# Kernel tuning notes

Measured on AMD Instinct MI355X. Metric: run time of the kernel, lower is better.

## Reference

```python
import jax, jax.numpy as jnp
import numpy as np

LN_EPS = 1e-5
MIN_BW, MAX_BW, BW_FACTOR = 0.1, 10.0, 1.0
BETA = 0.1


def _layernorm(h, g, b):
    mu = jnp.mean(h, axis=-1, keepdims=True)
    var = jnp.mean((h - mu) ** 2, axis=-1, keepdims=True)
    return (h - mu) * jax.lax.rsqrt(var + LN_EPS) * g + b


def _mlp(x, W1, b1, g, beta, W2, b2):
    # Linear -> LayerNorm -> Dropout(eval: identity) -> GELU(exact) -> Linear
    h = x @ W1 + b1
    h = _layernorm(h, g, beta)
    h = jax.nn.gelu(h, approximate=False)
    return h @ W2 + b2


def _normalize(x):
    n = jnp.linalg.norm(x, axis=-1, keepdims=True)
    return x / jnp.maximum(n, 1e-12)


def _bandwidth(x, y):
    # median-heuristic bandwidth on up to 512 samples; no grad through it
    s = min(512, x.shape[0])
    xs, ys = x[:s], y[:s]
    diff = xs[:, None, :] - ys[None, :, :]          # [s, s, K]
    dist_sq = jnp.sum(diff ** 2, axis=-1)
    bw = jnp.sqrt(jnp.median(dist_sq.reshape(-1)) / 2.0) * BW_FACTOR
    return jax.lax.stop_gradient(jnp.clip(bw, MIN_BW, MAX_BW))


def _score_kernel(x, sx, y, sy):
    # 3-term KSD kernel matrix [B, B]
    bw = _bandwidth(x, y)
    bw2 = bw ** 2
    x2 = jnp.sum(x ** 2, axis=-1)
    y2 = jnp.sum(y ** 2, axis=-1)
    dist_sq = jnp.maximum(x2[:, None] + y2[None, :] - 2.0 * (x @ y.T), 0.0)
    k = jnp.exp(-dist_sq / (2.0 * bw2))
    term1 = k * (sx @ sy.T)
    # sum_d (x_i - y_j)_d * sy_jd  = x_i . sy_j - y_j . sy_j
    term2 = (x @ sy.T - jnp.sum(y * sy, axis=-1)[None, :]) * k / bw2
    D = x.shape[-1]
    term3 = dist_sq * k / (bw2 ** 2) - k * D / bw2
    return term1 + term2 + term3


def setup_inputs() -> dict:
    key = jax.random.key(0)
    B, L, D1, H, K = 256, 128, 768, 1024, 256
    ks = jax.random.split(key, 16)

    def w(k, shape):
        return (jax.random.normal(k, shape, dtype=jnp.float32) * 0.02)

    inp = {
        'image_features': jax.random.normal(ks[0], (B, L, D1), dtype=jnp.float32),
        'text_features': jax.random.normal(ks[1], (B, L, D1), dtype=jnp.float32),
        'eps_img': jax.random.normal(ks[2], (B, L, K), dtype=jnp.float32),
        'eps_txt': jax.random.normal(ks[3], (B, L, K), dtype=jnp.float32),
        'attention_mask': jnp.ones((B, L), dtype=jnp.int32),
    }
    # encoders: D1 -> H -> 2K ; score nets: K -> 2K -> K
    for pfx, k1, k2 in (('enc_i', ks[4], ks[5]), ('enc_t', ks[6], ks[7])):
        inp[pfx + '_W1'] = w(k1, (D1, H)); inp[pfx + '_b1'] = jnp.zeros((H,), jnp.float32)
        inp[pfx + '_g'] = jnp.ones((H,), jnp.float32); inp[pfx + '_beta'] = jnp.zeros((H,), jnp.float32)
        inp[pfx + '_W2'] = w(k2, (H, 2 * K)); inp[pfx + '_b2'] = jnp.zeros((2 * K,), jnp.float32)
    for pfx, k1, k2 in (('sc_i', ks[8], ks[9]), ('sc_t', ks[10], ks[11])):
        inp[pfx + '_W1'] = w(k1, (K, 2 * K)); inp[pfx + '_b1'] = jnp.zeros((2 * K,), jnp.float32)
        inp[pfx + '_g'] = jnp.ones((2 * K,), jnp.float32); inp[pfx + '_beta'] = jnp.zeros((2 * K,), jnp.float32)
        inp[pfx + '_W2'] = w(k2, (2 * K, K)); inp[pfx + '_b2'] = jnp.zeros((K,), jnp.float32)
    return inp


def reference(image_features, text_features, attention_mask, eps_img, eps_txt,
              enc_i_W1, enc_i_b1, enc_i_g, enc_i_beta, enc_i_W2, enc_i_b2,
              enc_t_W1, enc_t_b1, enc_t_g, enc_t_beta, enc_t_W2, enc_t_b2,
              sc_i_W1, sc_i_b1, sc_i_g, sc_i_beta, sc_i_W2, sc_i_b2,
              sc_t_W1, sc_t_b1, sc_t_g, sc_t_beta, sc_t_W2, sc_t_b2):
    B = image_features.shape[0]
    img_params = _mlp(image_features, enc_i_W1, enc_i_b1, enc_i_g, enc_i_beta, enc_i_W2, enc_i_b2)
    txt_params = _mlp(text_features, enc_t_W1, enc_t_b1, enc_t_g, enc_t_beta, enc_t_W2, enc_t_b2)
    K = img_params.shape[-1] // 2
    img_mu, img_logvar = img_params[..., :K], img_params[..., K:]
    txt_mu, txt_logvar = txt_params[..., :K], txt_params[..., K:]

    img_z = _normalize(img_mu + eps_img * jnp.exp(0.5 * img_logvar))
    txt_z = _normalize(txt_mu + eps_txt * jnp.exp(0.5 * txt_logvar))

    img_score = _mlp(img_z, sc_i_W1, sc_i_b1, sc_i_g, sc_i_beta, sc_i_W2, sc_i_b2)
    txt_score = _mlp(txt_z, sc_t_W1, sc_t_b1, sc_t_g, sc_t_beta, sc_t_W2, sc_t_b2)

    seq_last = jnp.sum(attention_mask, axis=1).astype(jnp.int32) - 1   # [B]
    bidx = jnp.arange(B)
    xz, yz = img_z[bidx, seq_last], txt_z[bidx, seq_last]
    xs, ys = img_score[bidx, seq_last], txt_score[bidx, seq_last]

    alignment_loss = jnp.mean(_score_kernel(xz, xs, yz, ys))

    kl1 = -0.5 * jnp.sum(1.0 + img_logvar - img_mu ** 2 - jnp.exp(img_logvar), axis=-1)
    kl2 = -0.5 * jnp.sum(1.0 + txt_logvar - txt_mu ** 2 - jnp.exp(txt_logvar), axis=-1)
    kl_loss = (jnp.mean(kl1[bidx, seq_last]) + jnp.mean(kl2[bidx, seq_last])) / 2.0

    total_loss = kl_loss + BETA * alignment_loss
    return total_loss
```

## Files before the change

kernel.cpp:

```cpp
#include <hip/hip_runtime.h>
#include <math.h>

#define Bb   256
#define Lq   128
#define D1   768
#define Hh   1024
#define Kk   256
#define K2v  512

#define OFF_EPSG  0
#define OFF_P     131072
#define OFF_Z     4325376
#define OFF_SCORE 4456448
#define OFF_DIST  4587520
#define OFF_HIST  4653056
#define OFF_SCAL  4661248
#define OFF_YSY   4661256
#define OFF_BF    4661768

#define UB_XG   0
#define UB_HACT 393216
#define UB_ZB   917504
#define UB_WT   1048576
#define WT_EW1I 0
#define WT_EW1T 786432
#define WT_EW2I 1572864
#define WT_EW2T 2097152
#define WT_SW1I 2621440
#define WT_SW1T 2752512
#define WT_SW2I 2883584
#define WT_SW2T 3014656

typedef __attribute__((ext_vector_type(8))) short short8v;
typedef __attribute__((ext_vector_type(4))) float f32x4;

__device__ __forceinline__ float wred(float v){
#pragma unroll
  for (int m = 32; m; m >>= 1) v += __shfl_xor(v, m, 64);
  return v;
}
__device__ __forceinline__ int wredi(int v){
#pragma unroll
  for (int m = 32; m; m >>= 1) v += __shfl_xor(v, m, 64);
  return v;
}
__device__ __forceinline__ float gelu_exact(float x){
  return 0.5f * x * (1.0f + erff(x * 0.70710678118654752f));
}
__device__ __forceinline__ ushort f2b(float f){
  union { float f; unsigned u; } v; v.f = f;
  return (ushort)((v.u + 0x7FFFu + ((v.u >> 16) & 1u)) >> 16);
}

template<int BM,int KCH,int N,int K>
__device__ __forceinline__ void gemm_stage(
    const ushort* __restrict__ A, const ushort* __restrict__ WTi,
    const ushort* __restrict__ WTt, float* __restrict__ P,
    ushort* LS, int tid, int n0, int r0, int kb, int ks)
{
  constexpr int RPW = BM / 64;
  const int lane = tid & 63, wid = tid >> 6;
  const ushort* WT = (r0 >= 256) ? WTt : WTi;

  f32x4 acc[RPW][4];
#pragma unroll
  for (int s = 0; s < RPW; s++)
#pragma unroll
    for (int c = 0; c < 4; c++) acc[s][c] = (f32x4){0.f,0.f,0.f,0.f};

  const int l15 = lane & 15, kg = lane >> 4;
  const int rdswz = (kg * 16) ^ ((l15 & 3) << 4);

  for (int k0 = kb; k0 < kb + KCH; k0 += 32){
    __syncthreads();
    constexpr int NCHK = (BM + 64) * 4;
#pragma unroll
    for (int i = 0; i < NCHK / 256; i++){
      const int q = (i * 256 + tid) * 16;
      const int row = q >> 6, koff = q & 63;
      const ushort* src = (row < BM)
          ? (A  + (size_t)(r0 + row) * K + k0)
          : (WT + (size_t)(n0 + row - BM) * K + k0);
      short8v v = *reinterpret_cast<const short8v*>(
          reinterpret_cast<const char*>(src) + koff);
      const int dq = (q & ~63) | (koff ^ ((row & 3) << 4));
      *reinterpret_cast<short8v*>(reinterpret_cast<char*>(LS) + dq) = v;
    }
    __syncthreads();
    const char* Ab  = reinterpret_cast<const char*>(LS);
    const char* Bbp = reinterpret_cast<const char*>(LS + BM * 32);
    short8v ar[RPW], bc[4];
#pragma unroll
    for (int s = 0; s < RPW; s++){
      const int row = wid * (RPW * 16) + s * 16 + l15;
      ar[s] = *reinterpret_cast<const short8v*>(Ab + row * 64 + rdswz);
    }
#pragma unroll
    for (int c = 0; c < 4; c++){
      const int col = c * 16 + l15;
      bc[c] = *reinterpret_cast<const short8v*>(Bbp + col * 64 + rdswz);
    }
#pragma unroll
    for (int s = 0; s < RPW; s++)
#pragma unroll
      for (int c = 0; c < 4; c++)
        acc[s][c] = __builtin_amdgcn_mfma_f32_16x16x32_bf16(ar[s], bc[c], acc[s][c], 0, 0, 0);
  }
#pragma unroll
  for (int s = 0; s < RPW; s++)
#pragma unroll
    for (int c = 0; c < 4; c++)
#pragma unroll
      for (int r = 0; r < 4; r++){
        const int row = r0 + wid * (RPW * 16) + s * 16 + kg * 4 + r;
        const int col = n0 + c * 16 + l15;
        P[((size_t)ks * 512 + row) * N + col] = acc[s][c][r];
      }
}

template<int BM,int KCH,int N,int K>
__global__ __launch_bounds__(256) void k_mgemm(
    const ushort* __restrict__ A, const ushort* __restrict__ WTi,
    const ushort* __restrict__ WTt, float* __restrict__ P)
{
  __shared__ __align__(16) ushort LS[(BM + 64) * 32];
  gemm_stage<BM,KCH,N,K>(A, WTi, WTt, P, LS, threadIdx.x,
                         blockIdx.x * 64, blockIdx.y * BM,
                         blockIdx.z * KCH, blockIdx.z);
}

__global__ __launch_bounds__(256) void k_prep(
    const float* __restrict__ img, const float* __restrict__ txt,
    const float* __restrict__ epsi, const float* __restrict__ epst,
    const int* __restrict__ mask,
    const float* __restrict__ eW1i, const float* __restrict__ eW1t,
    const float* __restrict__ eW2i, const float* __restrict__ eW2t,
    const float* __restrict__ sW1i, const float* __restrict__ sW1t,
    const float* __restrict__ sW2i, const float* __restrict__ sW2t,
    ushort* __restrict__ xgb, float* __restrict__ epsg, ushort* __restrict__ wt,
    int* __restrict__ ghist, float* __restrict__ scal)
{
  __shared__ float lsf[32][33];
  __shared__ int s_last;
  const int bid = blockIdx.x, t = threadIdx.x;
  if (bid < 256){
    if (t < 8) reinterpret_cast<int4*>(ghist)[bid * 8 + t] = make_int4(0,0,0,0);
    if (bid == 0 && t < 8) scal[t] = 0.0f;
    int s = 0;
    if (t < 32){
      int4 v = reinterpret_cast<const int4*>(mask + bid * Lq)[t];
      s = v.x + v.y + v.z + v.w;
    }
    if (t < 64){
      int tot = wredi(s);
      if (t == 0) s_last = tot - 1;
    }
    __syncthreads();
    const int last = s_last;
    if (t < 192){
      float4 v = reinterpret_cast<const float4*>(img + (size_t)(bid*Lq+last)*D1)[t];
      ushort4 o; o.x=f2b(v.x); o.y=f2b(v.y); o.z=f2b(v.z); o.w=f2b(v.w);
      reinterpret_cast<ushort4*>(xgb + (size_t)bid*D1)[t] = o;
      float4 w = reinterpret_cast<const float4*>(txt + (size_t)(bid*Lq+last)*D1)[t];
      ushort4 q; q.x=f2b(w.x); q.y=f2b(w.y); q.z=f2b(w.z); q.w=f2b(w.w);
      reinterpret_cast<ushort4*>(xgb + (size_t)(Bb+bid)*D1)[t] = q;
    }
    if (t < 64){
      reinterpret_cast<float4*>(epsg + (size_t)bid*Kk)[t] =
        reinterpret_cast<const float4*>(epsi + (size_t)(bid*Lq+last)*Kk)[t];
      reinterpret_cast<float4*>(epsg + (size_t)(Bb+bid)*Kk)[t] =
        reinterpret_cast<const float4*>(epst + (size_t)(bid*Lq+last)*Kk)[t];
    }
    return;
  }
  const int wb = bid - 256;
  const float* src; ushort* dst; int Kd, Nd, ti;
  if      (wb < 768){  src=eW1i; dst=wt+WT_EW1I; Kd=768;  Nd=1024; ti=wb; }
  else if (wb < 1536){ src=eW1t; dst=wt+WT_EW1T; Kd=768;  Nd=1024; ti=wb-768; }
  else if (wb < 2048){ src=eW2i; dst=wt+WT_EW2I; Kd=1024; Nd=512;  ti=wb-1536; }
  else if (wb < 2560){ src=eW2t; dst=wt+WT_EW2T; Kd=1024; Nd=512;  ti=wb-2048; }
  else if (wb < 2688){ src=sW1i; dst=wt+WT_SW1I; Kd=256;  Nd=512;  ti=wb-2560; }
  else if (wb < 2816){ src=sW1t; dst=wt+WT_SW1T; Kd=256;  Nd=512;  ti=wb-2688; }
  else if (wb < 2944){ src=sW2i; dst=wt+WT_SW2I; Kd=512;  Nd=256;  ti=wb-2816; }
  else               { src=sW2t; dst=wt+WT_SW2T; Kd=512;  Nd=256;  ti=wb-2944; }
  const int ntile = Nd / 32;
  const int k0 = (ti / ntile) * 32, n0 = (ti % ntile) * 32;
  const int r = t >> 3, q = t & 7;
  float4 v = reinterpret_cast<const float4*>(src + (size_t)(k0+r)*Nd + n0)[q];
  lsf[r][q*4+0]=v.x; lsf[r][q*4+1]=v.y; lsf[r][q*4+2]=v.z; lsf[r][q*4+3]=v.w;
  __syncthreads();
  ushort4 o;
  o.x = f2b(lsf[q*4+0][r]); o.y = f2b(lsf[q*4+1][r]);
  o.z = f2b(lsf[q*4+2][r]); o.w = f2b(lsf[q*4+3][r]);
  *reinterpret_cast<ushort4*>(dst + (size_t)(n0+r)*Kd + k0 + q*4) = o;
}

template<int NS>
__global__ __launch_bounds__(256) void k_ln1(
    const float* __restrict__ P,
    const float* __restrict__ b1i, const float* __restrict__ b1t,
    const float* __restrict__ gi,  const float* __restrict__ gt,
    const float* __restrict__ bei, const float* __restrict__ bet,
    ushort* __restrict__ hb)
{
  __shared__ float2 wsum[4];
  const int row = blockIdx.x, t = threadIdx.x;
  const float* b1 = row >= 256 ? b1t : b1i;
  const float* g  = row >= 256 ? gt  : gi;
  const float* be = row >= 256 ? bet : bei;
  const float4* P4 = reinterpret_cast<const float4*>(P);
  float4 v = make_float4(0,0,0,0);
#pragma unroll
  for (int s = 0; s < NS; s++){
    float4 p = P4[((size_t)s * 512 + row) * (Hh/4) + t];
    v.x += p.x; v.y += p.y; v.z += p.z; v.w += p.w;
  }
  float4 bb = reinterpret_cast<const float4*>(b1)[t];
  v.x += bb.x; v.y += bb.y; v.z += bb.z; v.w += bb.w;
  float ps = wred(v.x + v.y + v.z + v.w);
  float pq = wred(v.x*v.x + v.y*v.y + v.z*v.z + v.w*v.w);
  if (!(t & 63)) wsum[t >> 6] = make_float2(ps, pq);
  __syncthreads();
  float S = 0, Q = 0;
#pragma unroll
  for (int i = 0; i < 4; i++){ S += wsum[i].x; Q += wsum[i].y; }
  float mean = S * (1.0f/Hh);
  float rstd = rsqrtf(Q * (1.0f/Hh) - mean*mean + 1e-5f);
  float4 gv  = reinterpret_cast<const float4*>(g)[t];
  float4 bev = reinterpret_cast<const float4*>(be)[t];
  ushort4 o;
  o.x = f2b(gelu_exact((v.x - mean)*rstd*gv.x + bev.x));
  o.y = f2b(gelu_exact((v.y - mean)*rstd*gv.y + bev.y));
  o.z = f2b(gelu_exact((v.z - mean)*rstd*gv.z + bev.z));
  o.w = f2b(gelu_exact((v.w - mean)*rstd*gv.w + bev.w));
  reinterpret_cast<ushort4*>(hb)[(size_t)row * 256 + t] = o;
}

template<int NS>
__global__ __launch_bounds__(128) void k_ln2(
    const float* __restrict__ P,
    const float* __restrict__ b1i, const float* __restrict__ b1t,
    const float* __restrict__ gi,  const float* __restrict__ gt,
    const float* __restrict__ bei, const float* __restrict__ bet,
    ushort* __restrict__ hb2)
{
  __shared__ float2 wsum[2];
  const int row = blockIdx.x, t = threadIdx.x;
  const float* b1 = row >= 256 ? b1t : b1i;
  const float* g  = row >= 256 ? gt  : gi;
  const float* be = row >= 256 ? bet : bei;
  const float4* P4 = reinterpret_cast<const float4*>(P);
  float4 v = make_float4(0,0,0,0);
#pragma unroll
  for (int s = 0; s < NS; s++){
    float4 p = P4[((size_t)s * 512 + row) * (K2v/4) + t];
    v.x += p.x; v.y += p.y; v.z += p.z; v.w += p.w;
  }
  float4 bb = reinterpret_cast<const float4*>(b1)[t];
  v.x += bb.x; v.y += bb.y; v.z += bb.z; v.w += bb.w;
  float ps = wred(v.x + v.y + v.z + v.w);
  float pq = wred(v.x*v.x + v.y*v.y + v.z*v.z + v.w*v.w);
  if (!(t & 63)) wsum[t >> 6] = make_float2(ps, pq);
  __syncthreads();
  float S = wsum[0].x + wsum[1].x, Q = wsum[0].y + wsum[1].y;
  float mean = S * (1.0f/K2v);
  float rstd = rsqrtf(Q * (1.0f/K2v) - mean*mean + 1e-5f);
  float4 gv  = reinterpret_cast<const float4*>(g)[t];
  float4 bev = reinterpret_cast<const float4*>(be)[t];
  ushort4 o;
  o.x = f2b(gelu_exact((v.x - mean)*rstd*gv.x + bev.x));
  o.y = f2b(gelu_exact((v.y - mean)*rstd*gv.y + bev.y));
  o.z = f2b(gelu_exact((v.z - mean)*rstd*gv.z + bev.z));
  o.w = f2b(gelu_exact((v.w - mean)*rstd*gv.w + bev.w));
  reinterpret_cast<ushort4*>(hb2)[(size_t)row * 128 + t] = o;
}

template<int NS>
__global__ __launch_bounds__(64) void k_reparam(
    const float* __restrict__ P,
    const float* __restrict__ b2i, const float* __restrict__ b2t,
    const float* __restrict__ epsg, float* __restrict__ z,
    ushort* __restrict__ zb, float* __restrict__ kl)
{
  const int row = blockIdx.x, t = threadIdx.x;
  const float* b2 = row >= 256 ? b2t : b2i;
  const float4* P4 = reinterpret_cast<const float4*>(P);
  float4 mu = make_float4(0,0,0,0), lv = make_float4(0,0,0,0);
#pragma unroll
  for (int s = 0; s < NS; s++){
    float4 a = P4[((size_t)s * 512 + row) * (K2v/4) + t];
    float4 c = P4[((size_t)s * 512 + row) * (K2v/4) + 64 + t];
    mu.x += a.x; mu.y += a.y; mu.z += a.z; mu.w += a.w;
    lv.x += c.x; lv.y += c.y; lv.z += c.z; lv.w += c.w;
  }
  float4 bm = reinterpret_cast<const float4*>(b2)[t];
  float4 bl = reinterpret_cast<const float4*>(b2)[64 + t];
  mu.x += bm.x; mu.y += bm.y; mu.z += bm.z; mu.w += bm.w;
  lv.x += bl.x; lv.y += bl.y; lv.z += bl.z; lv.w += bl.w;
  float4 ev = reinterpret_cast<const float4*>(epsg)[(size_t)row * 64 + t];
  float z0 = mu.x + ev.x * expf(0.5f * lv.x);
  float z1 = mu.y + ev.y * expf(0.5f * lv.y);
  float z2 = mu.z + ev.z * expf(0.5f * lv.z);
  float z3 = mu.w + ev.w * expf(0.5f * lv.w);
  float s2 = wred(z0*z0 + z1*z1 + z2*z2 + z3*z3);
  float klp = (1.0f + lv.x - mu.x*mu.x - expf(lv.x))
            + (1.0f + lv.y - mu.y*mu.y - expf(lv.y))
            + (1.0f + lv.z - mu.z*mu.z - expf(lv.z))
            + (1.0f + lv.w - mu.w*mu.w - expf(lv.w));
  float klt = wred(klp);
  float inv = 1.0f / fmaxf(sqrtf(s2), 1e-12f);
  float4 zv = make_float4(z0*inv, z1*inv, z2*inv, z3*inv);
  reinterpret_cast<float4*>(z)[(size_t)row * 64 + t] = zv;
  ushort4 o; o.x=f2b(zv.x); o.y=f2b(zv.y); o.z=f2b(zv.z); o.w=f2b(zv.w);
  reinterpret_cast<ushort4*>(zb)[(size_t)row * 64 + t] = o;
  if (t == 0) atomicAdd(kl + (row >= 256 ? 1 : 0), -0.5f * klt);
}

__global__ __launch_bounds__(256) void k_sc1dist(
    const ushort* __restrict__ zb, const ushort* __restrict__ WTi,
    const ushort* __restrict__ WTt, float* __restrict__ P,
    const float* __restrict__ z, float* __restrict__ dist, int* __restrict__ ghist)
{
  __shared__ __align__(16) char SM[256*4 + 8192*4];
  const int bid = blockIdx.x, t = threadIdx.x;
  if (bid < 256){
    ushort* LS = reinterpret_cast<ushort*>(SM);
    const int n0 = (bid & 7) * 64;
    const int r0 = ((bid >> 3) & 7) * 64;
    const int ks = bid >> 6;
    gemm_stage<64,64,512,256>(zb, WTi, WTt, P, LS, t, n0, r0, ks * 64, ks);
    return;
  }
  float* xsh = reinterpret_cast<float*>(SM);
  int*   hl  = reinterpret_cast<int*>(SM + 1024);
  const int i = bid - 256, j = t;
  xsh[j] = z[(size_t)i * Kk + j];
#pragma unroll
  for (int k = j; k < 8192; k += 256) hl[k] = 0;
  __syncthreads();
  const float4* y4 = reinterpret_cast<const float4*>(z + (size_t)Bb * Kk);
  const float4* x4 = reinterpret_cast<const float4*>(xsh);
  float acc = 0.0f;
#pragma unroll 4
  for (int d = 0; d < Kk; d += 4){
    float4 xv = x4[d >> 2];
    float4 yv = y4[j * (Kk/4) + (d >> 2)];
    float d0 = xv.x - yv.x, d1 = xv.y - yv.y, d2 = xv.z - yv.z, d3 = xv.w - yv.w;
    acc += d0*d0 + d1*d1 + d2*d2 + d3*d3;
  }
  dist[i * 256 + j] = acc;
  int bin = (int)(acc * 2048.0f);
  bin = bin < 0 ? 0 : (bin > 8191 ? 8191 : bin);
  atomicAdd(&hl[bin], 1);
  __syncthreads();
  for (int k = j; k < 8192; k += 256){
    int c = hl[k];
    if (c) atomicAdd(ghist + k, c);
  }
}

template<int NS>
__global__ __launch_bounds__(256) void k_sum2bw(
    const float* __restrict__ P,
    const float* __restrict__ b2i, const float* __restrict__ b2t,
    const float* __restrict__ z, float* __restrict__ score, float* __restrict__ ysy,
    const int* __restrict__ ghist, float* __restrict__ scal)
{
  const int bid = blockIdx.x, t = threadIdx.x;
  if (bid < 128){
    const int row = bid * 4 + (t >> 6), lane = t & 63;
    const float* b2 = row >= 256 ? b2t : b2i;
    const float4* P4 = reinterpret_cast<const float4*>(P);
    float4 v = make_float4(0,0,0,0);
#pragma unroll
    for (int s = 0; s < NS; s++){
      float4 q = P4[((size_t)s * 512 + row) * (Kk/4) + lane];
      v.x += q.x; v.y += q.y; v.z += q.z; v.w += q.w;
    }
    float4 bb = reinterpret_cast<const float4*>(b2)[lane];
    v.x += bb.x; v.y += bb.y; v.z += bb.z; v.w += bb.w;
    reinterpret_cast<float4*>(score)[(size_t)row * 64 + lane] = v;
    float4 zv = reinterpret_cast<const float4*>(z)[(size_t)row * 64 + lane];
    float yp = wred(zv.x*v.x + zv.y*v.y + zv.z*v.z + zv.w*v.w);
    if (lane == 0) ysy[row] = yp;
    return;
  }
  __shared__ int wt4[4];
  __shared__ int bres[2];
  const int lane = t & 63, w = t >> 6;
  const int base = t * 32;
  int s = 0;
#pragma unroll
  for (int u = 0; u < 32; u++) s += ghist[base + u];
  int sc = s;
#pragma unroll
  for (int m = 1; m < 64; m <<= 1){
    int o = __shfl_up(sc, m, 64);
    if (lane >= m) sc += o;
  }
  if (lane == 63) wt4[w] = sc;
  __syncthreads();
  int off = 0;
  for (int q = 0; q < w; q++) off += wt4[q];
  int cum = sc + off, basex = cum - s;
#pragma unroll
  for (int rr = 0; rr < 2; rr++){
    int rank = 32768 + rr;
    if (basex < rank && cum >= rank){
      int c = basex;
      for (int u = 0; u < 32; u++){
        c += ghist[base + u];
        if (c >= rank){ bres[rr] = base + u; break; }
      }
    }
  }
  __syncthreads();
  if (t == 0){
    float med = 0.5f * ((bres[0] + 0.5f) + (bres[1] + 0.5f)) * (1.0f / 2048.0f);
    float bw = sqrtf(med * 0.5f);
    bw = fminf(fmaxf(bw, 0.1f), 10.0f);
    scal[3] = bw * bw;
  }
}

__global__ __launch_bounds__(256) void k_score(
    const float* __restrict__ z, const float* __restrict__ score,
    const float* __restrict__ dist, const float* __restrict__ ysy,
    float* __restrict__ scal, float* __restrict__ out)
{
  __shared__ __align__(16) float xsh[Kk];
  __shared__ __align__(16) float sxsh[Kk];
  __shared__ float red4[4];
  const int i = blockIdx.x, j = threadIdx.x;
  xsh[j]  = z[(size_t)i * Kk + j];
  sxsh[j] = score[(size_t)i * Kk + j];
  __syncthreads();
  const float bw2 = scal[3];
  const float4* sy4 = reinterpret_cast<const float4*>(score + (size_t)Bb * Kk);
  const float4* x4  = reinterpret_cast<const float4*>(xsh);
  const float4* sx4 = reinterpret_cast<const float4*>(sxsh);
  float ssy = 0, xsy = 0;
#pragma unroll 4
  for (int d = 0; d < Kk; d += 4){
    float4 xv  = x4[d >> 2];
    float4 sxv = sx4[d >> 2];
    float4 syv = sy4[j * (Kk/4) + (d >> 2)];
    ssy += sxv.x*syv.x + sxv.y*syv.y + sxv.z*syv.z + sxv.w*syv.w;
    xsy += xv.x*syv.x + xv.y*syv.y + xv.z*syv.z + xv.w*syv.w;
  }
  float d2 = dist[i * 256 + j];
  float kv = expf(-d2 / (2.0f * bw2));
  float t1 = kv * ssy;
  float t2 = (xsy - ysy[Bb + j]) * kv / bw2;
  float t3 = d2 * kv / (bw2 * bw2) - kv * (float)Kk / bw2;
  float s = wred(t1 + t2 + t3);
  if (!(j & 63)) red4[j >> 6] = s;
  __syncthreads();
  if (j == 0){
    atomicAdd(scal + 2, red4[0] + red4[1] + red4[2] + red4[3]);
    __threadfence();
    int old = atomicAdd(reinterpret_cast<int*>(scal + 4), 1);
    if (old == 255){
      float kli = __int_as_float(atomicAdd(reinterpret_cast<int*>(scal + 0), 0));
      float klt = __int_as_float(atomicAdd(reinterpret_cast<int*>(scal + 1), 0));
      float alg = __int_as_float(atomicAdd(reinterpret_cast<int*>(scal + 2), 0));
      out[0] = 0.5f * (kli + klt) * (1.0f/256.0f) + 0.1f * alg * (1.0f/65536.0f);
    }
  }
}

extern "C" void kernel_launch(void* const* d_in, const int* in_sizes, int n_in,
                              void* d_out, int out_size, void* d_ws, size_t ws_size,
                              hipStream_t stream) {
  (void)in_sizes; (void)n_in; (void)out_size; (void)ws_size;
  const float* img  = (const float*)d_in[0];
  const float* txt  = (const float*)d_in[1];
  const float* epsi = (const float*)d_in[2];
  const float* epst = (const float*)d_in[3];
  const int*   mask = (const int*)d_in[4];
  const float* eW1i = (const float*)d_in[5];
  const float* eb1i = (const float*)d_in[6];
  const float* egi  = (const float*)d_in[7];
  const float* ebei = (const float*)d_in[8];
  const float* eW2i = (const float*)d_in[9];
  const float* eb2i = (const float*)d_in[10];
  const float* eW1t = (const float*)d_in[11];
  const float* eb1t = (const float*)d_in[12];
  const float* egt  = (const float*)d_in[13];
  const float* ebet = (const float*)d_in[14];
  const float* eW2t = (const float*)d_in[15];
  const float* eb2t = (const float*)d_in[16];
  const float* sW1i = (const float*)d_in[17];
  const float* sb1i = (const float*)d_in[18];
  const float* sgi  = (const float*)d_in[19];
  const float* sbei = (const float*)d_in[20];
  const float* sW2i = (const float*)d_in[21];
  const float* sb2i = (const float*)d_in[22];
  const float* sW1t = (const float*)d_in[23];
  const float* sb1t = (const float*)d_in[24];
  const float* sgt  = (const float*)d_in[25];
  const float* sbet = (const float*)d_in[26];
  const float* sW2t = (const float*)d_in[27];
  const float* sb2t = (const float*)d_in[28];

  float*  ws    = (float*)d_ws;
  float*  epsg  = ws + OFF_EPSG;
  float*  P     = ws + OFF_P;
  float*  z     = ws + OFF_Z;
  float*  score = ws + OFF_SCORE;
  float*  dist  = ws + OFF_DIST;
  int*    ghist = (int*)(ws + OFF_HIST);
  float*  scal  = ws + OFF_SCAL;
  float*  ysy   = ws + OFF_YSY;
  ushort* ub    = (ushort*)(ws + OFF_BF);
  ushort* xgb   = ub + UB_XG;
  ushort* hb    = ub + UB_HACT;
  ushort* zb    = ub + UB_ZB;
  ushort* wt    = ub + UB_WT;

  k_prep<<<3328, 256, 0, stream>>>(img, txt, epsi, epst, mask,
                                   eW1i, eW1t, eW2i, eW2t,
                                   sW1i, sW1t, sW2i, sW2t,
                                   xgb, epsg, wt, ghist, scal);
  k_mgemm<128,96,1024,768><<<dim3(16,4,8), 256, 0, stream>>>(xgb, wt+WT_EW1I, wt+WT_EW1T, P);
  k_ln1<8><<<512, 256, 0, stream>>>(P, eb1i, eb1t, egi, egt, ebei, ebet, hb);
  k_mgemm<128,64,512,1024><<<dim3(8,4,16), 256, 0, stream>>>(hb, wt+WT_EW2I, wt+WT_EW2T, P);
  k_reparam<16><<<512, 64, 0, stream>>>(P, eb2i, eb2t, epsg, z, zb, scal);
  k_sc1dist<<<512, 256, 0, stream>>>(zb, wt+WT_SW1I, wt+WT_SW1T, P, z, dist, ghist);
  k_ln2<4><<<512, 128, 0, stream>>>(P, sb1i, sb1t, sgi, sgt, sbei, sbet, hb);
  k_mgemm<64,32,256,512><<<dim3(4,8,16), 256, 0, stream>>>(hb, wt+WT_SW2I, wt+WT_SW2T, P);
  k_sum2bw<16><<<129, 256, 0, stream>>>(P, sb2i, sb2t, z, score, ysy, ghist, scal);
  k_score<<<256, 256, 0, stream>>>(z, score, dist, ysy, scal, (float*)d_out);
}
```

Measured before the change: 94.48 us.

## Fuse split-K GEMMs with LayerNorm, reparam and score-net epilogues into row-block kernels

Replaces the split-K MFMA GEMMs and their separate partial-sum reduction and LayerNorm/GELU kernels with fused kernels. Each block owns 16 full rows, computes the whole output width in registers, and applies bias, LayerNorm, GELU, reparameterisation/KL or the second score-net layer in shared memory. The bandwidth median search is folded into k_score, and the P workspace is removed, so there are fewer launches and no round trips of fp32 partial sums through global memory. In exchange only 32 blocks run the GEMM stages, and B operands are read straight from global memory without LDS staging, which risks low occupancy and latency-bound inner loops.

Result: slower. 158.2 us (+67.5%).

```diff
diff --git a/kernel.cpp b/kernel.cpp
--- a/kernel.cpp
+++ b/kernel.cpp
@@ -9,14 +9,13 @@
 #define K2v  512
 
 #define OFF_EPSG  0
-#define OFF_P     131072
-#define OFF_Z     4325376
-#define OFF_SCORE 4456448
-#define OFF_DIST  4587520
-#define OFF_HIST  4653056
-#define OFF_SCAL  4661248
-#define OFF_YSY   4661256
-#define OFF_BF    4661768
+#define OFF_Z     131072
+#define OFF_SCORE 262144
+#define OFF_DIST  393216
+#define OFF_HIST  458752
+#define OFF_SCAL  466944
+#define OFF_YSY   466952
+#define OFF_BF    467464
 
 #define UB_XG   0
 #define UB_HACT 393216
@@ -50,83 +49,6 @@
 __device__ __forceinline__ ushort f2b(float f){
   union { float f; unsigned u; } v; v.f = f;
   return (ushort)((v.u + 0x7FFFu + ((v.u >> 16) & 1u)) >> 16);
-}
-
-template<int BM,int KCH,int N,int K>
-__device__ __forceinline__ void gemm_stage(
-    const ushort* __restrict__ A, const ushort* __restrict__ WTi,
-    const ushort* __restrict__ WTt, float* __restrict__ P,
-    ushort* LS, int tid, int n0, int r0, int kb, int ks)
-{
-  constexpr int RPW = BM / 64;
-  const int lane = tid & 63, wid = tid >> 6;
-  const ushort* WT = (r0 >= 256) ? WTt : WTi;
-
-  f32x4 acc[RPW][4];
-#pragma unroll
-  for (int s = 0; s < RPW; s++)
-#pragma unroll
-    for (int c = 0; c < 4; c++) acc[s][c] = (f32x4){0.f,0.f,0.f,0.f};
-
-  const int l15 = lane & 15, kg = lane >> 4;
-  const int rdswz = (kg * 16) ^ ((l15 & 3) << 4);
-
-  for (int k0 = kb; k0 < kb + KCH; k0 += 32){
-    __syncthreads();
-    constexpr int NCHK = (BM + 64) * 4;
-#pragma unroll
-    for (int i = 0; i < NCHK / 256; i++){
-      const int q = (i * 256 + tid) * 16;
-      const int row = q >> 6, koff = q & 63;
-      const ushort* src = (row < BM)
-          ? (A  + (size_t)(r0 + row) * K + k0)
-          : (WT + (size_t)(n0 + row - BM) * K + k0);
-      short8v v = *reinterpret_cast<const short8v*>(
-          reinterpret_cast<const char*>(src) + koff);
-      const int dq = (q & ~63) | (koff ^ ((row & 3) << 4));
-      *reinterpret_cast<short8v*>(reinterpret_cast<char*>(LS) + dq) = v;
-    }
-    __syncthreads();
-    const char* Ab  = reinterpret_cast<const char*>(LS);
-    const char* Bbp = reinterpret_cast<const char*>(LS + BM * 32);
-    short8v ar[RPW], bc[4];
-#pragma unroll
-    for (int s = 0; s < RPW; s++){
-      const int row = wid * (RPW * 16) + s * 16 + l15;
-      ar[s] = *reinterpret_cast<const short8v*>(Ab + row * 64 + rdswz);
-    }
-#pragma unroll
-    for (int c = 0; c < 4; c++){
-      const int col = c * 16 + l15;
-      bc[c] = *reinterpret_cast<const short8v*>(Bbp + col * 64 + rdswz);
-    }
-#pragma unroll
-    for (int s = 0; s < RPW; s++)
-#pragma unroll
-      for (int c = 0; c < 4; c++)
-        acc[s][c] = __builtin_amdgcn_mfma_f32_16x16x32_bf16(ar[s], bc[c], acc[s][c], 0, 0, 0);
-  }
-#pragma unroll
-  for (int s = 0; s < RPW; s++)
-#pragma unroll
-    for (int c = 0; c < 4; c++)
-#pragma unroll
-      for (int r = 0; r < 4; r++){
-        const int row = r0 + wid * (RPW * 16) + s * 16 + kg * 4 + r;
-        const int col = n0 + c * 16 + l15;
-        P[((size_t)ks * 512 + row) * N + col] = acc[s][c][r];
-      }
-}
-
-template<int BM,int KCH,int N,int K>
-__global__ __launch_bounds__(256) void k_mgemm(
-    const ushort* __restrict__ A, const ushort* __restrict__ WTi,
-    const ushort* __restrict__ WTt, float* __restrict__ P)
-{
-  __shared__ __align__(16) ushort LS[(BM + 64) * 32];
-  gemm_stage<BM,KCH,N,K>(A, WTi, WTt, P, LS, threadIdx.x,
-                         blockIdx.x * 64, blockIdx.y * BM,
-                         blockIdx.z * KCH, blockIdx.z);
 }
 
 __global__ __launch_bounds__(256) void k_prep(
@@ -195,247 +117,348 @@
   *reinterpret_cast<ushort4*>(dst + (size_t)(n0+r)*Kd + k0 + q*4) = o;
 }
 
-template<int NS>
-__global__ __launch_bounds__(256) void k_ln1(
-    const float* __restrict__ P,
+__global__ __launch_bounds__(1024) void k_enc1(
+    const ushort* __restrict__ xgb,
+    const ushort* __restrict__ WTi, const ushort* __restrict__ WTt,
     const float* __restrict__ b1i, const float* __restrict__ b1t,
     const float* __restrict__ gi,  const float* __restrict__ gt,
     const float* __restrict__ bei, const float* __restrict__ bet,
     ushort* __restrict__ hb)
 {
-  __shared__ float2 wsum[4];
-  const int row = blockIdx.x, t = threadIdx.x;
-  const float* b1 = row >= 256 ? b1t : b1i;
-  const float* g  = row >= 256 ? gt  : gi;
-  const float* be = row >= 256 ? bet : bei;
-  const float4* P4 = reinterpret_cast<const float4*>(P);
-  float4 v = make_float4(0,0,0,0);
-#pragma unroll
-  for (int s = 0; s < NS; s++){
-    float4 p = P4[((size_t)s * 512 + row) * (Hh/4) + t];
-    v.x += p.x; v.y += p.y; v.z += p.z; v.w += p.w;
-  }
-  float4 bb = reinterpret_cast<const float4*>(b1)[t];
-  v.x += bb.x; v.y += bb.y; v.z += bb.z; v.w += bb.w;
-  float ps = wred(v.x + v.y + v.z + v.w);
-  float pq = wred(v.x*v.x + v.y*v.y + v.z*v.z + v.w*v.w);
-  if (!(t & 63)) wsum[t >> 6] = make_float2(ps, pq);
-  __syncthreads();
-  float S = 0, Q = 0;
-#pragma unroll
-  for (int i = 0; i < 4; i++){ S += wsum[i].x; Q += wsum[i].y; }
-  float mean = S * (1.0f/Hh);
-  float rstd = rsqrtf(Q * (1.0f/Hh) - mean*mean + 1e-5f);
-  float4 gv  = reinterpret_cast<const float4*>(g)[t];
-  float4 bev = reinterpret_cast<const float4*>(be)[t];
-  ushort4 o;
-  o.x = f2b(gelu_exact((v.x - mean)*rstd*gv.x + bev.x));
-  o.y = f2b(gelu_exact((v.y - mean)*rstd*gv.y + bev.y));
-  o.z = f2b(gelu_exact((v.z - mean)*rstd*gv.z + bev.z));
-  o.w = f2b(gelu_exact((v.w - mean)*rstd*gv.w + bev.w));
-  reinterpret_cast<ushort4*>(hb)[(size_t)row * 256 + t] = o;
-}
-
-template<int NS>
-__global__ __launch_bounds__(128) void k_ln2(
-    const float* __restrict__ P,
-    const float* __restrict__ b1i, const float* __restrict__ b1t,
-    const float* __restrict__ gi,  const float* __restrict__ gt,
-    const float* __restrict__ bei, const float* __restrict__ bet,
-    ushort* __restrict__ hb2)
+  __shared__ __align__(16) char ALS[16 * 768 * 2];
+  __shared__ float Hf[16][1028];
+  const int tid = threadIdx.x, lane = tid & 63, w = tid >> 6;
+  const int r0 = blockIdx.x * 16;
+  const ushort* WT = (r0 >= 256) ? WTt : WTi;
+  const float* b1 = (r0 >= 256) ? b1t : b1i;
+  const float* g  = (r0 >= 256) ? gt  : gi;
+  const float* be = (r0 >= 256) ? bet : bei;
+
+  for (int q = tid; q < 16 * 96; q += 1024){
+    int m = q / 96, k8 = q % 96;
+    short8v v = *reinterpret_cast<const short8v*>(xgb + (size_t)(r0+m)*D1 + k8*8);
+    int dq = ((k8 >> 2)*16 + m)*64 + (((k8 & 3) << 4) ^ ((m & 3) << 4));
+    *reinterpret_cast<short8v*>(ALS + dq) = v;
+  }
+  __syncthreads();
+  const int l15 = lane & 15, kg = lane >> 4;
+  const int cb = w * 64;
+  f32x4 acc[4];
+#pragma unroll
+  for (int c = 0; c < 4; c++) acc[c] = (f32x4){0.f,0.f,0.f,0.f};
+#pragma unroll 2
+  for (int ks = 0; ks < 24; ks++){
+    short8v av = *reinterpret_cast<const short8v*>(
+        ALS + (ks*16 + l15)*64 + ((kg*16) ^ ((l15 & 3) << 4)));
+#pragma unroll
+    for (int c = 0; c < 4; c++){
+      short8v bv = *reinterpret_cast<const short8v*>(
+          WT + (size_t)(cb + c*16 + l15)*D1 + ks*32 + kg*8);
+      acc[c] = __builtin_amdgcn_mfma_f32_16x16x32_bf16(av, bv, acc[c], 0, 0, 0);
+    }
+  }
+#pragma unroll
+  for (int c = 0; c < 4; c++){
+    const int col = cb + c*16 + l15;
+    const float bv = b1[col];
+#pragma unroll
+    for (int r = 0; r < 4; r++) Hf[kg*4 + r][col] = acc[c][r] + bv;
+  }
+  __syncthreads();
+  float s = 0.f, q2 = 0.f;
+#pragma unroll
+  for (int j = 0; j < 16; j++){
+    float x = Hf[w][lane + 64*j];
+    s += x; q2 += x*x;
+  }
+  s = wred(s); q2 = wred(q2);
+  const float mean = s * (1.0f/1024.0f);
+  const float rstd = rsqrtf(q2 * (1.0f/1024.0f) - mean*mean + 1e-5f);
+  const int c0 = lane * 16;
+  short8v o0, o1;
+#pragma unroll
+  for (int j = 0; j < 8; j++){
+    float x0 = (Hf[w][c0+j]   - mean)*rstd*g[c0+j]   + be[c0+j];
+    float x1 = (Hf[w][c0+8+j] - mean)*rstd*g[c0+8+j] + be[c0+8+j];
+    o0[j] = (short)f2b(gelu_exact(x0));
+    o1[j] = (short)f2b(gelu_exact(x1));
+  }
+  *reinterpret_cast<short8v*>(hb + (size_t)(r0+w)*Hh + c0)     = o0;
+  *reinterpret_cast<short8v*>(hb + (size_t)(r0+w)*Hh + c0 + 8) = o1;
+}
+
+__global__ __launch_bounds__(512) void k_enc2(
+    const ushort* __restrict__ hbA,
+    const ushort* __restrict__ WTi, const ushort* __restrict__ WTt,
+    const float* __restrict__ b2i, const float* __restrict__ b2t,
+    const float* __restrict__ epsg,
+    float* __restrict__ z, ushort* __restrict__ zb, float* __restrict__ kl)
 {
-  __shared__ float2 wsum[2];
-  const int row = blockIdx.x, t = threadIdx.x;
-  const float* b1 = row >= 256 ? b1t : b1i;
-  const float* g  = row >= 256 ? gt  : gi;
-  const float* be = row >= 256 ? bet : bei;
-  const float4* P4 = reinterpret_cast<const float4*>(P);
-  float4 v = make_float4(0,0,0,0);
-#pragma unroll
-  for (int s = 0; s < NS; s++){
-    float4 p = P4[((size_t)s * 512 + row) * (K2v/4) + t];
-    v.x += p.x; v.y += p.y; v.z += p.z; v.w += p.w;
-  }
-  float4 bb = reinterpret_cast<const float4*>(b1)[t];
-  v.x += bb.x; v.y += bb.y; v.z += bb.z; v.w += bb.w;
-  float ps = wred(v.x + v.y + v.z + v.w);
-  float pq = wred(v.x*v.x + v.y*v.y + v.z*v.z + v.w*v.w);
-  if (!(t & 63)) wsum[t >> 6] = make_float2(ps, pq);
-  __syncthreads();
-  float S = wsum[0].x + wsum[1].x, Q = wsum[0].y + wsum[1].y;
-  float mean = S * (1.0f/K2v);
-  float rstd = rsqrtf(Q * (1.0f/K2v) - mean*mean + 1e-5f);
-  float4 gv  = reinterpret_cast<const float4*>(g)[t];
-  float4 bev = reinterpret_cast<const float4*>(be)[t];
-  ushort4 o;
-  o.x = f2b(gelu_exact((v.x - mean)*rstd*gv.x + bev.x));
-  o.y = f2b(gelu_exact((v.y - mean)*rstd*gv.y + bev.y));
-  o.z = f2b(gelu_exact((v.z - mean)*rstd*gv.z + bev.z));
-  o.w = f2b(gelu_exact((v.w - mean)*rstd*gv.w + bev.w));
-  reinterpret_cast<ushort4*>(hb2)[(size_t)row * 128 + t] = o;
-}
-
-template<int NS>
-__global__ __launch_bounds__(64) void k_reparam(
-    const float* __restrict__ P,
-    const float* __restrict__ b2i, const float* __restrict__ b2t,
-    const float* __restrict__ epsg, float* __restrict__ z,
-    ushort* __restrict__ zb, float* __restrict__ kl)
+  __shared__ __align__(16) char ALS[16 * 1024 * 2];
+  __shared__ float Hf[16][516];
+  const int tid = threadIdx.x, lane = tid & 63, w = tid >> 6;
+  const int r0 = blockIdx.x * 16;
+  const ushort* WT = (r0 >= 256) ? WTt : WTi;
+  const float* b2 = (r0 >= 256) ? b2t : b2i;
+
+  for (int q = tid; q < 16 * 128; q += 512){
+    int m = q >> 7, k8 = q & 127;
+    short8v v = *reinterpret_cast<const short8v*>(hbA + (size_t)(r0+m)*Hh + k8*8);
+    int dq = ((k8 >> 2)*16 + m)*64 + (((k8 & 3) << 4) ^ ((m & 3) << 4));
+    *reinterpret_cast<short8v*>(ALS + dq) = v;
+  }
+  __syncthreads();
+  const int l15 = lane & 15, kg = lane >> 4;
+  const int cb = w * 64;
+  f32x4 acc[4];
+#pragma unroll
+  for (int c = 0; c < 4; c++) acc[c] = (f32x4){0.f,0.f,0.f,0.f};
+#pragma unroll 2
+  for (int ks = 0; ks < 32; ks++){
+    short8v av = *reinterpret_cast<const short8v*>(
+        ALS + (ks*16 + l15)*64 + ((kg*16) ^ ((l15 & 3) << 4)));
+#pragma unroll
+    for (int c = 0; c < 4; c++){
+      short8v bv = *reinterpret_cast<const short8v*>(
+          WT + (size_t)(cb + c*16 + l15)*Hh + ks*32 + kg*8);
+      acc[c] = __builtin_amdgcn_mfma_f32_16x16x32_bf16(av, bv, acc[c], 0, 0, 0);
+    }
+  }
+#pragma unroll
+  for (int c = 0; c < 4; c++){
+    const int col = cb + c*16 + l15;
+    const float bv = b2[col];
+#pragma unroll
+    for (int r = 0; r < 4; r++) Hf[kg*4 + r][col] = acc[c][r] + bv;
+  }
+  __syncthreads();
+#pragma unroll
+  for (int rr = 0; rr < 2; rr++){
+    const int row = w + rr*8;
+    const int grow = r0 + row;
+    float4 mu = *reinterpret_cast<const float4*>(&Hf[row][lane*4]);
+    float4 lv = *reinterpret_cast<const float4*>(&Hf[row][256 + lane*4]);
+    float4 ev = reinterpret_cast<const float4*>(epsg + (size_t)grow*Kk)[lane];
+    float z0 = mu.x + ev.x * expf(0.5f * lv.x);
+    float z1 = mu.y + ev.y * expf(0.5f * lv.y);
+    float z2 = mu.z + ev.z * expf(0.5f * lv.z);
+    float z3 = mu.w + ev.w * expf(0.5f * lv.w);
+    float s2 = wred(z0*z0 + z1*z1 + z2*z2 + z3*z3);
+    float klp = (1.0f + lv.x - mu.x*mu.x - expf(lv.x))
+              + (1.0f + lv.y - mu.y*mu.y - expf(lv.y))
+              + (1.0f + lv.z - mu.z*mu.z - expf(lv.z))
+              + (1.0f + lv.w - mu.w*mu.w - expf(lv.w));
+    float klt = wred(klp);
+    float inv = 1.0f / fmaxf(sqrtf(s2), 1e-12f);
+    float4 zv = make_float4(z0*inv, z1*inv, z2*inv, z3*inv);
+    reinterpret_cast<float4*>(z)[(size_t)grow * 64 + lane] = zv;
+    ushort4 o; o.x=f2b(zv.x); o.y=f2b(zv.y); o.z=f2b(zv.z); o.w=f2b(zv.w);
+    reinterpret_cast<ushort4*>(zb)[(size_t)grow * 64 + lane] = o;
+    if (lane == 0) atomicAdd(kl + (grow >= 256 ? 1 : 0), -0.5f * klt);
+  }
+}
+
+__global__ __launch_bounds__(512) void k_sc(
+    const ushort* __restrict__ zb,
+    const ushort* __restrict__ W1i, const ushort* __restrict__ W1t,
+    const float* __restrict__ sb1i, const float* __restrict__ sb1t,
+    const float* __restrict__ sgi,  const float* __restrict__ sgt,
+    const float* __restrict__ sbei, const float* __restrict__ sbet,
+    const ushort* __restrict__ W2i, const ushort* __restrict__ W2t,
+    const float* __restrict__ sb2i, const float* __restrict__ sb2t,
+    const float* __restrict__ z, float* __restrict__ score, float* __restrict__ ysy,
+    float* __restrict__ dist, int* __restrict__ ghist)
 {
-  const int row = blockIdx.x, t = threadIdx.x;
-  const float* b2 = row >= 256 ? b2t : b2i;
-  const float4* P4 = reinterpret_cast<const float4*>(P);
-  float4 mu = make_float4(0,0,0,0), lv = make_float4(0,0,0,0);
-#pragma unroll
-  for (int s = 0; s < NS; s++){
-    float4 a = P4[((size_t)s * 512 + row) * (K2v/4) + t];
-    float4 c = P4[((size_t)s * 512 + row) * (K2v/4) + 64 + t];
-    mu.x += a.x; mu.y += a.y; mu.z += a.z; mu.w += a.w;
-    lv.x += c.x; lv.y += c.y; lv.z += c.z; lv.w += c.w;
-  }
-  float4 bm = reinterpret_cast<const float4*>(b2)[t];
-  float4 bl = reinterpret_cast<const float4*>(b2)[64 + t];
-  mu.x += bm.x; mu.y += bm.y; mu.z += bm.z; mu.w += bm.w;
-  lv.x += bl.x; lv.y += bl.y; lv.z += bl.z; lv.w += bl.w;
-  float4 ev = reinterpret_cast<const float4*>(epsg)[(size_t)row * 64 + t];
-  float z0 = mu.x + ev.x * expf(0.5f * lv.x);
-  float z1 = mu.y + ev.y * expf(0.5f * lv.y);
-  float z2 = mu.z + ev.z * expf(0.5f * lv.z);
-  float z3 = mu.w + ev.w * expf(0.5f * lv.w);
-  float s2 = wred(z0*z0 + z1*z1 + z2*z2 + z3*z3);
-  float klp = (1.0f + lv.x - mu.x*mu.x - expf(lv.x))
-            + (1.0f + lv.y - mu.y*mu.y - expf(lv.y))
-            + (1.0f + lv.z - mu.z*mu.z - expf(lv.z))
-            + (1.0f + lv.w - mu.w*mu.w - expf(lv.w));
-  float klt = wred(klp);
-  float inv = 1.0f / fmaxf(sqrtf(s2), 1e-12f);
-  float4 zv = make_float4(z0*inv, z1*inv, z2*inv, z3*inv);
-  reinterpret_cast<float4*>(z)[(size_t)row * 64 + t] = zv;
-  ushort4 o; o.x=f2b(zv.x); o.y=f2b(zv.y); o.z=f2b(zv.z); o.w=f2b(zv.w);
-  reinterpret_cast<ushort4*>(zb)[(size_t)row * 64 + t] = o;
-  if (t == 0) atomicAdd(kl + (row >= 256 ? 1 : 0), -0.5f * klt);
-}
-
-__global__ __launch_bounds__(256) void k_sc1dist(
-    const ushort* __restrict__ zb, const ushort* __restrict__ WTi,
-    const ushort* __restrict__ WTt, float* __restrict__ P,
-    const float* __restrict__ z, float* __restrict__ dist, int* __restrict__ ghist)
-{
-  __shared__ __align__(16) char SM[256*4 + 8192*4];
-  const int bid = blockIdx.x, t = threadIdx.x;
-  if (bid < 256){
-    ushort* LS = reinterpret_cast<ushort*>(SM);
-    const int n0 = (bid & 7) * 64;
-    const int r0 = ((bid >> 3) & 7) * 64;
-    const int ks = bid >> 6;
-    gemm_stage<64,64,512,256>(zb, WTi, WTt, P, LS, t, n0, r0, ks * 64, ks);
+  __shared__ __align__(16) char SM[74240];
+  const int bid = blockIdx.x, tid = threadIdx.x;
+  const int lane = tid & 63, w = tid >> 6;
+  if (bid < 32){
+    char* ALS = SM;
+    float (*Hf)[516] = reinterpret_cast<float(*)[516]>(SM + 8192);
+    char* HK = SM + 8192 + 33024;
+    float (*SF)[260] = reinterpret_cast<float(*)[260]>(SM + 57600);
+    const int r0 = bid * 16;
+    const ushort* W1 = (r0 >= 256) ? W1t : W1i;
+    const float* b1 = (r0 >= 256) ? sb1t : sb1i;
+    const float* g  = (r0 >= 256) ? sgt  : sgi;
+    const float* be = (r0 >= 256) ? sbet : sbei;
+    const ushort* W2 = (r0 >= 256) ? W2t : W2i;
+    const float* b2 = (r0 >= 256) ? sb2t : sb2i;
+
+    {
+      int q = tid;
+      int m = q >> 5, k8 = q & 31;
+      short8v v = *reinterpret_cast<const short8v*>(zb + (size_t)(r0+m)*Kk + k8*8);
+      int dq = ((k8 >> 2)*16 + m)*64 + (((k8 & 3) << 4) ^ ((m & 3) << 4));
+      *reinterpret_cast<short8v*>(ALS + dq) = v;
+    }
+    __syncthreads();
+    const int l15 = lane & 15, kg = lane >> 4;
+    {
+      const int cb = w * 64;
+      f32x4 acc[4];
+#pragma unroll
+      for (int c = 0; c < 4; c++) acc[c] = (f32x4){0.f,0.f,0.f,0.f};
+#pragma unroll
+      for (int ks = 0; ks < 8; ks++){
+        short8v av = *reinterpret_cast<const short8v*>(
+            ALS + (ks*16 + l15)*64 + ((kg*16) ^ ((l15 & 3) << 4)));
+#pragma unroll
+        for (int c = 0; c < 4; c++){
+          short8v bv = *reinterpret_cast<const short8v*>(
+              W1 + (size_t)(cb + c*16 + l15)*Kk + ks*32 + kg*8);
+          acc[c] = __builtin_amdgcn_mfma_f32_16x16x32_bf16(av, bv, acc[c], 0, 0, 0);
+        }
+      }
+#pragma unroll
+      for (int c = 0; c < 4; c++){
+        const int col = cb + c*16 + l15;
+        const float bv = b1[col];
+#pragma unroll
+        for (int r = 0; r < 4; r++) Hf[kg*4 + r][col] = acc[c][r] + bv;
+      }
+    }
+    __syncthreads();
+#pragma unroll
+    for (int rr = 0; rr < 2; rr++){
+      const int row = w + rr*8;
+      float s = 0.f, q2 = 0.f;
+#pragma unroll
+      for (int j = 0; j < 8; j++){
+        float x = Hf[row][lane + 64*j];
+        s += x; q2 += x*x;
+      }
+      s = wred(s); q2 = wred(q2);
+      const float mean = s * (1.0f/512.0f);
+      const float rstd = rsqrtf(q2 * (1.0f/512.0f) - mean*mean + 1e-5f);
+      const int c0 = lane * 8;
+      short8v o;
+#pragma unroll
+      for (int j = 0; j < 8; j++){
+        float x = (Hf[row][c0+j] - mean)*rstd*g[c0+j] + be[c0+j];
+        o[j] = (short)f2b(gelu_exact(x));
+      }
+      int dq = ((lane >> 2)*16 + row)*64 + (((lane & 3) << 4) ^ ((row & 3) << 4));
+      *reinterpret_cast<short8v*>(HK + dq) = o;
+    }
+    __syncthreads();
+    {
+      const int cw = w * 32;
+      f32x4 acc[2];
+      acc[0] = (f32x4){0.f,0.f,0.f,0.f}; acc[1] = (f32x4){0.f,0.f,0.f,0.f};
+#pragma unroll 2
+      for (int ks = 0; ks < 16; ks++){
+        short8v av = *reinterpret_cast<const short8v*>(
+            HK + (ks*16 + l15)*64 + ((kg*16) ^ ((l15 & 3) << 4)));
+#pragma unroll
+        for (int c = 0; c < 2; c++){
+          short8v bv = *reinterpret_cast<const short8v*>(
+              W2 + (size_t)(cw + c*16 + l15)*K2v + ks*32 + kg*8);
+          acc[c] = __builtin_amdgcn_mfma_f32_16x16x32_bf16(av, bv, acc[c], 0, 0, 0);
+        }
+      }
+#pragma unroll
+      for (int c = 0; c < 2; c++){
+        const int col = cw + c*16 + l15;
+        const float bv = b2[col];
+#pragma unroll
+        for (int r = 0; r < 4; r++) SF[kg*4 + r][col] = acc[c][r] + bv;
+      }
+    }
+    __syncthreads();
+#pragma unroll
+    for (int rr = 0; rr < 2; rr++){
+      const int row = w + rr*8;
+      const int grow = r0 + row;
+      float4 sv = *reinterpret_cast<const float4*>(&SF[row][lane*4]);
+      reinterpret_cast<float4*>(score)[(size_t)grow * 64 + lane] = sv;
+      float4 zv = reinterpret_cast<const float4*>(z)[(size_t)grow * 64 + lane];
+      float yp = wred(zv.x*sv.x + zv.y*sv.y + zv.z*sv.z + zv.w*sv.w);
+      if (lane == 0) ysy[grow] = yp;
+    }
     return;
   }
-  float* xsh = reinterpret_cast<float*>(SM);
-  int*   hl  = reinterpret_cast<int*>(SM + 1024);
-  const int i = bid - 256, j = t;
-  xsh[j] = z[(size_t)i * Kk + j];
-#pragma unroll
-  for (int k = j; k < 8192; k += 256) hl[k] = 0;
+  float (*xsh)[256] = reinterpret_cast<float(*)[256]>(SM);
+  int* hl = reinterpret_cast<int*>(SM + 2048);
+  const int ti = tid >> 8, tt = tid & 255;
+  const int i = (bid - 32) * 2 + ti;
+  xsh[ti][tt] = z[(size_t)i * Kk + tt];
+  for (int k = tid; k < 8192; k += 512) hl[k] = 0;
   __syncthreads();
   const float4* y4 = reinterpret_cast<const float4*>(z + (size_t)Bb * Kk);
-  const float4* x4 = reinterpret_cast<const float4*>(xsh);
+  const float4* x4 = reinterpret_cast<const float4*>(xsh[ti]);
   float acc = 0.0f;
 #pragma unroll 4
   for (int d = 0; d < Kk; d += 4){
     float4 xv = x4[d >> 2];
-    float4 yv = y4[j * (Kk/4) + (d >> 2)];
+    float4 yv = y4[tt * (Kk/4) + (d >> 2)];
     float d0 = xv.x - yv.x, d1 = xv.y - yv.y, d2 = xv.z - yv.z, d3 = xv.w - yv.w;
     acc += d0*d0 + d1*d1 + d2*d2 + d3*d3;
   }
-  dist[i * 256 + j] = acc;
+  dist[i * 256 + tt] = acc;
   int bin = (int)(acc * 2048.0f);
   bin = bin < 0 ? 0 : (bin > 8191 ? 8191 : bin);
   atomicAdd(&hl[bin], 1);
   __syncthreads();
-  for (int k = j; k < 8192; k += 256){
+  for (int k = tid; k < 8192; k += 512){
     int c = hl[k];
     if (c) atomicAdd(ghist + k, c);
-  }
-}
-
-template<int NS>
-__global__ __launch_bounds__(256) void k_sum2bw(
-    const float* __restrict__ P,
-    const float* __restrict__ b2i, const float* __restrict__ b2t,
-    const float* __restrict__ z, float* __restrict__ score, float* __restrict__ ysy,
-    const int* __restrict__ ghist, float* __restrict__ scal)
-{
-  const int bid = blockIdx.x, t = threadIdx.x;
-  if (bid < 128){
-    const int row = bid * 4 + (t >> 6), lane = t & 63;
-    const float* b2 = row >= 256 ? b2t : b2i;
-    const float4* P4 = reinterpret_cast<const float4*>(P);
-    float4 v = make_float4(0,0,0,0);
-#pragma unroll
-    for (int s = 0; s < NS; s++){
-      float4 q = P4[((size_t)s * 512 + row) * (Kk/4) + lane];
-      v.x += q.x; v.y += q.y; v.z += q.z; v.w += q.w;
-    }
-    float4 bb = reinterpret_cast<const float4*>(b2)[lane];
-    v.x += bb.x; v.y += bb.y; v.z += bb.z; v.w += bb.w;
-    reinterpret_cast<float4*>(score)[(size_t)row * 64 + lane] = v;
-    float4 zv = reinterpret_cast<const float4*>(z)[(size_t)row * 64 + lane];
-    float yp = wred(zv.x*v.x + zv.y*v.y + zv.z*v.z + zv.w*v.w);
-    if (lane == 0) ysy[row] = yp;
-    return;
-  }
-  __shared__ int wt4[4];
-  __shared__ int bres[2];
-  const int lane = t & 63, w = t >> 6;
-  const int base = t * 32;
-  int s = 0;
-#pragma unroll
-  for (int u = 0; u < 32; u++) s += ghist[base + u];
-  int sc = s;
-#pragma unroll
-  for (int m = 1; m < 64; m <<= 1){
-    int o = __shfl_up(sc, m, 64);
-    if (lane >= m) sc += o;
-  }
-  if (lane == 63) wt4[w] = sc;
-  __syncthreads();
-  int off = 0;
-  for (int q = 0; q < w; q++) off += wt4[q];
-  int cum = sc + off, basex = cum - s;
-#pragma unroll
-  for (int rr = 0; rr < 2; rr++){
-    int rank = 32768 + rr;
-    if (basex < rank && cum >= rank){
-      int c = basex;
-      for (int u = 0; u < 32; u++){
-        c += ghist[base + u];
-        if (c >= rank){ bres[rr] = base + u; break; }
-      }
-    }
-  }
-  __syncthreads();
-  if (t == 0){
-    float med = 0.5f * ((bres[0] + 0.5f) + (bres[1] + 0.5f)) * (1.0f / 2048.0f);
-    float bw = sqrtf(med * 0.5f);
-    bw = fminf(fmaxf(bw, 0.1f), 10.0f);
-    scal[3] = bw * bw;
   }
 }
 
 __global__ __launch_bounds__(256) void k_score(
     const float* __restrict__ z, const float* __restrict__ score,
     const float* __restrict__ dist, const float* __restrict__ ysy,
-    float* __restrict__ scal, float* __restrict__ out)
+    const int* __restrict__ ghist, float* __restrict__ scal,
+    float* __restrict__ out)
 {
   __shared__ __align__(16) float xsh[Kk];
   __shared__ __align__(16) float sxsh[Kk];
+  __shared__ int wt4[4];
+  __shared__ int bres[2];
   __shared__ float red4[4];
+  __shared__ float s_bw2;
   const int i = blockIdx.x, j = threadIdx.x;
   xsh[j]  = z[(size_t)i * Kk + j];
   sxsh[j] = score[(size_t)i * Kk + j];
-  __syncthreads();
-  const float bw2 = scal[3];
+  {
+    const int lane = j & 63, w = j >> 6;
+    const int base = j * 32;
+    int s = 0;
+#pragma unroll
+    for (int u = 0; u < 32; u++) s += ghist[base + u];
+    int sc = s;
+#pragma unroll
+    for (int m = 1; m < 64; m <<= 1){
+      int o = __shfl_up(sc, m, 64);
+      if (lane >= m) sc += o;
+    }
+    if (lane == 63) wt4[w] = sc;
+    __syncthreads();
+    int off = 0;
+    for (int q = 0; q < w; q++) off += wt4[q];
+    int cum = sc + off, basex = cum - s;
+#pragma unroll
+    for (int rr = 0; rr < 2; rr++){
+      int rank = 32768 + rr;
+      if (basex < rank && cum >= rank){
+        int c = basex;
+        for (int u = 0; u < 32; u++){
+          c += ghist[base + u];
+          if (c >= rank){ bres[rr] = base + u; break; }
+        }
+      }
+    }
+    __syncthreads();
+    if (j == 0){
+      float med = 0.5f * ((bres[0] + 0.5f) + (bres[1] + 0.5f)) * (1.0f / 2048.0f);
+      float bw = sqrtf(med * 0.5f);
+      bw = fminf(fmaxf(bw, 0.1f), 10.0f);
+      s_bw2 = bw * bw;
+    }
+    __syncthreads();
+  }
+  const float bw2 = s_bw2;
   const float4* sy4 = reinterpret_cast<const float4*>(score + (size_t)Bb * Kk);
   const float4* x4  = reinterpret_cast<const float4*>(xsh);
   const float4* sx4 = reinterpret_cast<const float4*>(sxsh);
@@ -505,7 +528,6 @@
 
   float*  ws    = (float*)d_ws;
   float*  epsg  = ws + OFF_EPSG;
-  float*  P     = ws + OFF_P;
   float*  z     = ws + OFF_Z;
   float*  score = ws + OFF_SCORE;
   float*  dist  = ws + OFF_DIST;
@@ -522,13 +544,13 @@
                                    eW1i, eW1t, eW2i, eW2t,
                                    sW1i, sW1t, sW2i, sW2t,
                                    xgb, epsg, wt, ghist, scal);
-  k_mgemm<128,96,1024,768><<<dim3(16,4,8), 256, 0, stream>>>(xgb, wt+WT_EW1I, wt+WT_EW1T, P);
-  k_ln1<8><<<512, 256, 0, stream>>>(P, eb1i, eb1t, egi, egt, ebei, ebet, hb);
-  k_mgemm<128,64,512,1024><<<dim3(8,4,16), 256, 0, stream>>>(hb, wt+WT_EW2I, wt+WT_EW2T, P);
-  k_reparam<16><<<512, 64, 0, stream>>>(P, eb2i, eb2t, epsg, z, zb, scal);
-  k_sc1dist<<<512, 256, 0, stream>>>(zb, wt+WT_SW1I, wt+WT_SW1T, P, z, dist, ghist);
-  k_ln2<4><<<512, 128, 0, stream>>>(P, sb1i, sb1t, sgi, sgt, sbei, sbet, hb);
-  k_mgemm<64,32,256,512><<<dim3(4,8,16), 256, 0, stream>>>(hb, wt+WT_SW2I, wt+WT_SW2T, P);
-  k_sum2bw<16><<<129, 256, 0, stream>>>(P, sb2i, sb2t, z, score, ysy, ghist, scal);
-  k_score<<<256, 256, 0, stream>>>(z, score, dist, ysy, scal, (float*)d_out);
-}
+  k_enc1<<<32, 1024, 0, stream>>>(xgb, wt+WT_EW1I, wt+WT_EW1T,
+                                  eb1i, eb1t, egi, egt, ebei, ebet, hb);
+  k_enc2<<<32, 512, 0, stream>>>(hb, wt+WT_EW2I, wt+WT_EW2T,
+                                 eb2i, eb2t, epsg, z, zb, scal);
+  k_sc<<<160, 512, 0, stream>>>(zb, wt+WT_SW1I, wt+WT_SW1T,
+                                sb1i, sb1t, sgi, sgt, sbei, sbet,
+                                wt+WT_SW2I, wt+WT_SW2T, sb2i, sb2t,
+                                z, score, ysy, dist, ghist);
+  k_score<<<256, 256, 0, stream>>>(z, score, dist, ysy, ghist, scal, (float*)d_out);
+}
```
